# Optimization experiments

Measured on AMD Instinct MI355X. Metric: run time of the kernel, lower is better.

The kernel has to match this reference:

```python
import jax, jax.numpy as jnp
import numpy as np

B, H, S, D = 4, 16, 2048, 128


def setup_inputs() -> dict:
    key = jax.random.key(0)
    kq, kk, kv = jax.random.split(key, 3)
    query = jax.random.normal(kq, (B, H, S, D), dtype=jnp.float32)
    key_t = jax.random.normal(kk, (B, H, S, D), dtype=jnp.float32)
    value = jax.random.normal(kv, (B, H, S, D), dtype=jnp.float32)
    # causal mask, broadcast over batch and heads: True = keep
    mask = jnp.tril(jnp.ones((S, S), dtype=bool))[None, None].repeat(B, 0).repeat(H, 1)
    return {"query": query, "key": key_t, "value": value, "mask": mask}


def reference(query, key, value, mask):
    scale = 1.0 / np.sqrt(D).astype(np.float32)
    # [b,h,sq,sk] scores
    scores = jnp.einsum("bhqd,bhkd->bhqk", query, key) * scale
    scores = jnp.where(mask, scores, -jnp.inf)
    probs = jax.nn.softmax(scores, axis=-1)
    return jnp.einsum("bhqk,bhkd->bhqd", probs, value)
```

## Files before the change

### kernel.cpp

```cpp
#include <hip/hip_runtime.h>


#define SLEN 2048
#define DDIM 128
#define NBH  64
#define QB   256
#define KB   64

typedef __bf16 bf16x8 __attribute__((ext_vector_type(8)));
typedef float  f32x16 __attribute__((ext_vector_type(16)));
typedef float  f32x4  __attribute__((ext_vector_type(4)));
typedef unsigned uint32x4 __attribute__((ext_vector_type(4)));
typedef unsigned short ushort_t;
typedef ushort_t ushort8 __attribute__((ext_vector_type(8)));

__device__ inline ushort_t f2bf(float f) {
  union { float f; unsigned u; } v; v.f = f;
  unsigned u = v.u;
  u += 0x7FFFu + ((u >> 16) & 1u);
  return (ushort_t)(u >> 16);
}

__device__ inline unsigned cvtpk_bf16(float lo, float hi) {
  unsigned r;
  asm("v_cvt_pk_bf16_f32 %0, %1, %2" : "=v"(r) : "v"(lo), "v"(hi));
  return r;
}

__global__ __launch_bounds__(256) void convert_k_kernel(
    const float* __restrict__ in, ushort_t* __restrict__ out, int n4) {
  int stride = gridDim.x * blockDim.x;
  for (int i = blockIdx.x * blockDim.x + threadIdx.x; i < n4; i += stride) {
    float4 x = reinterpret_cast<const float4*>(in)[i];
    unsigned lo = (unsigned)f2bf(x.x) | ((unsigned)f2bf(x.y) << 16);
    unsigned hi = (unsigned)f2bf(x.z) | ((unsigned)f2bf(x.w) << 16);
    reinterpret_cast<uint2*>(out)[i] = make_uint2(lo, hi);
  }
}

__global__ __launch_bounds__(256) void transpose_v_kernel(
    const float* __restrict__ V, ushort_t* __restrict__ Vt) {
  __shared__ float t[64][33];
  const int bh = blockIdx.z;
  const int s0 = blockIdx.x * 64;
  const int d0 = blockIdx.y * 32;
  const int tx = threadIdx.x & 31;
  const int ty = threadIdx.x >> 5;
  const float* src = V + ((size_t)bh * SLEN + s0) * DDIM + d0;
#pragma unroll
  for (int j = 0; j < 8; ++j) {
    int sl = ty + j * 8;
    t[sl][tx] = src[(size_t)sl * DDIM + tx];
  }
  __syncthreads();
  ushort_t* dst = Vt + ((size_t)bh * DDIM + d0) * SLEN + s0;
#pragma unroll
  for (int j = 0; j < 4; ++j) {
    int dl = ty + j * 8;
    unsigned lo = f2bf(t[tx * 2][dl]);
    unsigned hi = f2bf(t[tx * 2 + 1][dl]);
    *reinterpret_cast<unsigned*>(&dst[(size_t)dl * SLEN + tx * 2]) =
        lo | (hi << 16);
  }
}

__global__ __launch_bounds__(512, 2) void fattn3_kernel(
    const float* __restrict__ Q, const ushort_t* __restrict__ Kb,
    const ushort_t* __restrict__ Vt, float* __restrict__ Out) {
  __shared__ ushort_t K_sh[2][KB * DDIM];
  __shared__ ushort_t V_sh[2][DDIM * KB];

  const int tid  = threadIdx.x;
  const int lane = tid & 63;
  const int wv   = tid >> 6;
  const int l31  = lane & 31;
  const int hi   = lane >> 5;
  const int qblk = (blockIdx.y >= 32) ? blockIdx.x : (7 - (int)blockIdx.x);
  const int bh   = blockIdx.y;

  const float scale = 0.08838834764831845f;

  const float*    Qp = Q  + (size_t)bh * SLEN * DDIM;
  const ushort_t* Kp = Kb + (size_t)bh * SLEN * DDIM;
  const ushort_t* Vp = Vt + (size_t)bh * DDIM * SLEN;
  float*          Op = Out + (size_t)bh * SLEN * DDIM;

  const int q0w = qblk * QB + wv * 32;
  const int qg  = q0w + l31;

  bf16x8 qf[8];
  {
    const float* qr = Qp + (size_t)qg * DDIM;
#pragma unroll
    for (int ds = 0; ds < 8; ++ds) {
      int d0 = ds * 16 + hi * 8;
      float4 x = *reinterpret_cast<const float4*>(qr + d0);
      float4 y = *reinterpret_cast<const float4*>(qr + d0 + 4);
      ushort8 uu;
      uu[0] = f2bf(x.x * scale); uu[1] = f2bf(x.y * scale);
      uu[2] = f2bf(x.z * scale); uu[3] = f2bf(x.w * scale);
      uu[4] = f2bf(y.x * scale); uu[5] = f2bf(y.y * scale);
      uu[6] = f2bf(y.z * scale); uu[7] = f2bf(y.w * scale);
      qf[ds] = __builtin_bit_cast(bf16x8, uu);
    }
  }

  f32x16 Oacc[4];
#pragma unroll
  for (int dt = 0; dt < 4; ++dt)
#pragma unroll
    for (int r = 0; r < 16; ++r) Oacc[dt][r] = 0.f;
  float m_run = -3.0e38f, l_run = 0.f;

  const int last_kb      = qblk * 4 + 3;
  const int last_kb_wave = (q0w + 31) >> 6;

  auto stage = [&](int buf, int kb) {
    const ushort_t* ksrc = Kp + (size_t)kb * KB * DDIM;
#pragma unroll
    for (int j = 0; j < 2; ++j) {
      int chunk = wv * 128 + j * 64 + lane;
      int row = chunk >> 4, c = chunk & 15;
      const ushort_t* g = ksrc + row * DDIM + ((c ^ (row & 7)) << 3);
      ushort_t* l = &K_sh[buf][(size_t)(wv * 128 + j * 64) * 8];
      __builtin_amdgcn_global_load_lds(
          (const __attribute__((address_space(1))) unsigned*)g,
          (__attribute__((address_space(3))) unsigned*)l, 16, 0, 0);
    }
    const ushort_t* vsrc = Vp + (size_t)kb * KB;
#pragma unroll
    for (int j = 0; j < 2; ++j) {
      int chunk = wv * 128 + j * 64 + lane;
      int row = chunk >> 3, c = chunk & 7;
      const ushort_t* g = vsrc + (size_t)row * SLEN + ((c ^ (row & 7)) << 3);
      ushort_t* l = &V_sh[buf][(size_t)(wv * 128 + j * 64) * 8];
      __builtin_amdgcn_global_load_lds(
          (const __attribute__((address_space(1))) unsigned*)g,
          (__attribute__((address_space(3))) unsigned*)l, 16, 0, 0);
    }
  };

  stage(0, 0);

  for (int kb = 0; kb <= last_kb; ++kb) {
    __syncthreads();
    if (kb < last_kb) stage((kb + 1) & 1, kb + 1);

    if (kb <= last_kb_wave) {
      const int buf = kb & 1;

      f32x16 sac[2];
#pragma unroll
      for (int mt = 0; mt < 2; ++mt) {
        f32x16 a;
#pragma unroll
        for (int r = 0; r < 16; ++r) a[r] = 0.f;
        int row = mt * 32 + l31;
        int sw = row & 7;
#pragma unroll
        for (int ds = 0; ds < 8; ++ds) {
          int c = ds * 2 + hi;
          bf16x8 kf = *reinterpret_cast<const bf16x8*>(
              &K_sh[buf][row * DDIM + ((c ^ sw) << 3)]);
          a = __builtin_amdgcn_mfma_f32_32x32x16_bf16(kf, qf[ds], a, 0, 0, 0);
        }
        sac[mt] = a;
      }

      if (kb * 64 + 63 > q0w) {
#pragma unroll
        for (int mt = 0; mt < 2; ++mt) {
          int kbase = kb * 64 + mt * 32 + 4 * hi;
#pragma unroll
          for (int r = 0; r < 16; ++r) {
            int krow = (r & 3) + 8 * (r >> 2);
            if (kbase + krow > qg) sac[mt][r] = -3.0e38f;
          }
        }
      }

      float tm = sac[0][0];
#pragma unroll
      for (int r = 1; r < 16; ++r) tm = fmaxf(tm, sac[0][r]);
#pragma unroll
      for (int r = 0; r < 16; ++r) tm = fmaxf(tm, sac[1][r]);
      tm = fmaxf(tm, __shfl_xor(tm, 32));

      if (!__all(tm <= m_run)) {
        float mnew  = fmaxf(m_run, tm);
        float alpha = __expf(m_run - mnew);
        m_run = mnew;
        l_run *= alpha;
#pragma unroll
        for (int dt = 0; dt < 4; ++dt)
#pragma unroll
          for (int r = 0; r < 16; ++r) Oacc[dt][r] *= alpha;
      }

      float rs = 0.f;
#pragma unroll
      for (int mt = 0; mt < 2; ++mt)
#pragma unroll
        for (int r = 0; r < 16; ++r) {
          float p = __expf(sac[mt][r] - m_run);
          sac[mt][r] = p;
          rs += p;
        }
      rs += __shfl_xor(rs, 32);
      l_run += rs;

      uint32x4 pw[4];
#pragma unroll
      for (int ks = 0; ks < 4; ++ks) {
        const int mt = ks >> 1;
        const int hb = 4 * 2 * (ks & 1);
        unsigned pk_h0_0 = cvtpk_bf16(sac[mt][hb + 0], sac[mt][hb + 1]);
        unsigned pk_h0_1 = cvtpk_bf16(sac[mt][hb + 2], sac[mt][hb + 3]);
        unsigned pk_h1_0 = cvtpk_bf16(sac[mt][hb + 4], sac[mt][hb + 5]);
        unsigned pk_h1_1 = cvtpk_bf16(sac[mt][hb + 6], sac[mt][hb + 7]);
        unsigned s0 = hi ? pk_h1_0 : pk_h0_0;
        unsigned s1 = hi ? pk_h1_1 : pk_h0_1;
        unsigned t0 = hi ? pk_h0_0 : pk_h1_0;
        unsigned t1 = hi ? pk_h0_1 : pk_h1_1;
        unsigned r0 = __shfl_xor(t0, 32);
        unsigned r1 = __shfl_xor(t1, 32);
        uint32x4 f;
        f.x = hi ? r0 : s0;
        f.y = hi ? r1 : s1;
        f.z = hi ? s0 : r0;
        f.w = hi ? s1 : r1;
        pw[ks] = f;
      }

#pragma unroll
      for (int dt = 0; dt < 4; ++dt) {
        int row = dt * 32 + l31;
        int sw = row & 7;
#pragma unroll
        for (int ks = 0; ks < 4; ++ks) {
          int c = ks * 2 + hi;
          bf16x8 vf = *reinterpret_cast<const bf16x8*>(
              &V_sh[buf][row * 64 + ((c ^ sw) << 3)]);
          Oacc[dt] = __builtin_amdgcn_mfma_f32_32x32x16_bf16(
              vf, __builtin_bit_cast(bf16x8, pw[ks]), Oacc[dt], 0, 0, 0);
        }
      }
    }
  }

  {
    float invl = 1.0f / l_run;
    float* orow = Op + (size_t)qg * DDIM;
#pragma unroll
    for (int dt = 0; dt < 4; ++dt)
#pragma unroll
      for (int r = 0; r < 16; ++r) {
        int d = dt * 32 + (r & 3) + 8 * (r >> 2) + 4 * hi;
        orow[d] = Oacc[dt][r] * invl;
      }
  }
}

__global__ __launch_bounds__(256) void fattn_kernel(
    const float* __restrict__ Q, const float* __restrict__ K,
    const float* __restrict__ V, float* __restrict__ Out) {
  __shared__ ushort_t K_sh[64 * 128];
  __shared__ ushort_t V_sh[128 * 64];
  __shared__ ushort_t P_sh[4][16 * 64];

  const int tid  = threadIdx.x;
  const int lane = tid & 63;
  const int wv   = tid >> 6;
  const int l16  = lane & 15;
  const int lhi  = lane >> 4;
  const int qblk = blockIdx.x;
  const int bh   = blockIdx.y;
  const float scale = 0.08838834764831845f;

  const size_t base = (size_t)bh * SLEN * DDIM;
  const float* Qp = Q + base;
  const float* Kp = K + base;
  const float* Vp = V + base;
  float*       Op = Out + base;

  bf16x8 qf[4];
  {
    const int qrow = qblk * 64 + wv * 16 + l16;
    const float* qr = Qp + (size_t)qrow * DDIM;
#pragma unroll
    for (int dc = 0; dc < 4; ++dc) {
      int d0 = dc * 32 + lhi * 8;
      float4 x = *reinterpret_cast<const float4*>(qr + d0);
      float4 y = *reinterpret_cast<const float4*>(qr + d0 + 4);
      ushort8 uu;
      uu[0] = f2bf(x.x * scale); uu[1] = f2bf(x.y * scale);
      uu[2] = f2bf(x.z * scale); uu[3] = f2bf(x.w * scale);
      uu[4] = f2bf(y.x * scale); uu[5] = f2bf(y.y * scale);
      uu[6] = f2bf(y.z * scale); uu[7] = f2bf(y.w * scale);
      qf[dc] = __builtin_bit_cast(bf16x8, uu);
    }
  }

  f32x4 Oacc[8];
#pragma unroll
  for (int i = 0; i < 8; ++i) Oacc[i] = (f32x4){0.f, 0.f, 0.f, 0.f};
  float m_run[4], l_run[4];
#pragma unroll
  for (int r = 0; r < 4; ++r) { m_run[r] = -3.0e38f; l_run[r] = 0.f; }

  for (int kb = 0; kb <= qblk; ++kb) {
    __syncthreads();
    {
      const float* src = Kp + (size_t)kb * 64 * DDIM;
#pragma unroll
      for (int it = 0; it < 8; ++it) {
        int idx4 = it * 256 + tid;
        int r  = idx4 >> 5;
        int c4 = idx4 & 31;
        float4 x = *reinterpret_cast<const float4*>(src + r * DDIM + c4 * 4);
        unsigned lo = ((unsigned)f2bf(x.y) << 16) | f2bf(x.x);
        unsigned hh = ((unsigned)f2bf(x.w) << 16) | f2bf(x.z);
        int e = (r * 128 + c4 * 4) ^ ((r & 7) << 3);
        *reinterpret_cast<uint2*>(&K_sh[e]) = make_uint2(lo, hh);
      }
      const float* vs = Vp + (size_t)kb * 64 * DDIM;
#pragma unroll
      for (int it = 0; it < 8; ++it) {
        int idx4 = it * 256 + tid;
        int r  = idx4 >> 5;
        int c4 = idx4 & 31;
        float4 x = *reinterpret_cast<const float4*>(vs + r * DDIM + c4 * 4);
        int c0 = c4 * 4;
        float vals[4] = {x.x, x.y, x.z, x.w};
#pragma unroll
        for (int j = 0; j < 4; ++j) {
          int d = c0 + j;
          V_sh[(d * 64 + r) ^ ((d & 7) << 3)] = f2bf(vals[j]);
        }
      }
    }
    __syncthreads();

    f32x4 sacc[4];
#pragma unroll
    for (int g = 0; g < 4; ++g) {
      f32x4 acc = (f32x4){0.f, 0.f, 0.f, 0.f};
#pragma unroll
      for (int dc = 0; dc < 4; ++dc) {
        int row = g * 16 + l16;
        int e = (row * 128 + dc * 32 + lhi * 8) ^ ((row & 7) << 3);
        bf16x8 kf = *reinterpret_cast<const bf16x8*>(&K_sh[e]);
        acc = __builtin_amdgcn_mfma_f32_16x16x32_bf16(qf[dc], kf, acc, 0, 0, 0);
      }
      sacc[g] = acc;
    }

    if (kb == qblk) {
      int q0 = lhi * 4;
#pragma unroll
      for (int g = 0; g < 4; ++g) {
        int kcol = g * 16 + l16;
#pragma unroll
        for (int r = 0; r < 4; ++r) {
          if (kcol > wv * 16 + q0 + r) sacc[g][r] = -3.0e38f;
        }
      }
    }

    float tmax[4];
#pragma unroll
    for (int r = 0; r < 4; ++r)
      tmax[r] = fmaxf(fmaxf(sacc[0][r], sacc[1][r]),
                      fmaxf(sacc[2][r], sacc[3][r]));
#pragma unroll
    for (int x = 1; x < 16; x <<= 1) {
#pragma unroll
      for (int r = 0; r < 4; ++r)
        tmax[r] = fmaxf(tmax[r], __shfl_xor(tmax[r], x));
    }

    float alpha[4], mnew[4];
#pragma unroll
    for (int r = 0; r < 4; ++r) {
      mnew[r]  = fmaxf(m_run[r], tmax[r]);
      alpha[r] = __expf(m_run[r] - mnew[r]);
      m_run[r] = mnew[r];
    }

    float rsum[4] = {0.f, 0.f, 0.f, 0.f};
#pragma unroll
    for (int g = 0; g < 4; ++g) {
#pragma unroll
      for (int r = 0; r < 4; ++r) {
        float p = __expf(sacc[g][r] - mnew[r]);
        rsum[r] += p;
        int prow = lhi * 4 + r;
        P_sh[wv][(prow * 64 + g * 16 + l16) ^ ((prow & 7) << 3)] = f2bf(p);
      }
    }
#pragma unroll
    for (int x = 1; x < 16; x <<= 1) {
#pragma unroll
      for (int r = 0; r < 4; ++r) rsum[r] += __shfl_xor(rsum[r], x);
    }
#pragma unroll
    for (int r = 0; r < 4; ++r) l_run[r] = l_run[r] * alpha[r] + rsum[r];

#pragma unroll
    for (int dg = 0; dg < 8; ++dg)
#pragma unroll
      for (int r = 0; r < 4; ++r) Oacc[dg][r] *= alpha[r];

    bf16x8 pf[2];
#pragma unroll
    for (int kc = 0; kc < 2; ++kc) {
      int e = (l16 * 64 + kc * 32 + lhi * 8) ^ ((l16 & 7) << 3);
      pf[kc] = *reinterpret_cast<const bf16x8*>(&P_sh[wv][e]);
    }
#pragma unroll
    for (int dg = 0; dg < 8; ++dg) {
#pragma unroll
      for (int kc = 0; kc < 2; ++kc) {
        int row = dg * 16 + l16;
        int e = (row * 64 + kc * 32 + lhi * 8) ^ ((row & 7) << 3);
        bf16x8 vf = *reinterpret_cast<const bf16x8*>(&V_sh[e]);
        Oacc[dg] = __builtin_amdgcn_mfma_f32_16x16x32_bf16(pf[kc], vf, Oacc[dg], 0, 0, 0);
      }
    }
  }

#pragma unroll
  for (int r = 0; r < 4; ++r) {
    float inv = 1.0f / l_run[r];
    int q = qblk * 64 + wv * 16 + lhi * 4 + r;
    float* orow = Op + (size_t)q * DDIM;
#pragma unroll
    for (int dg = 0; dg < 8; ++dg)
      orow[dg * 16 + l16] = Oacc[dg][r] * inv;
  }
}

extern "C" void kernel_launch(void* const* d_in, const int* in_sizes, int n_in,
                              void* d_out, int out_size, void* d_ws, size_t ws_size,
                              hipStream_t stream) {
  const float* Q = (const float*)d_in[0];
  const float* K = (const float*)d_in[1];
  const float* V = (const float*)d_in[2];
  float* O = (float*)d_out;

  const size_t n_elem = (size_t)NBH * SLEN * DDIM;
  const size_t need   = n_elem * 2 * 2;

  if (ws_size >= need) {
    ushort_t* Kbf = (ushort_t*)d_ws;
    ushort_t* Vt  = Kbf + n_elem;
    convert_k_kernel<<<2048, 256, 0, stream>>>(K, Kbf, (int)(n_elem / 4));
    transpose_v_kernel<<<dim3(SLEN / 64, DDIM / 32, NBH), 256, 0, stream>>>(V, Vt);
    fattn3_kernel<<<dim3(SLEN / QB, NBH), dim3(512), 0, stream>>>(Q, Kbf, Vt, O);
  } else {
    fattn_kernel<<<dim3(SLEN / 64, NBH), dim3(256), 0, stream>>>(Q, K, V, O);
  }
}
```

Measured before the change: 149.8 us.

## Use exp2 with folded log2e scale, lazy rescale, permlane swap, MFMA priority

Folds log2(e) into the Q scale so the softmax can call the raw v_exp_f32 (exp2) instruction instead of __expf. The running-max rescale of the output accumulators is skipped unless the new max exceeds the old one by more than a threshold. It also replaces the cross-half shuffle used to pack P with v_permlane32_swap, splits the max and sum reductions into four independent chains, and raises wave priority around the MFMA loops. The lazy rescale risks fp32 overflow headroom issues if scores jump by less than the threshold repeatedly, but the bound keeps the exponentials at most 2^11.

Result: faster. 143.1 us (-4.5%).

```diff
diff --git a/kernel.cpp b/kernel.cpp
--- a/kernel.cpp
+++ b/kernel.cpp
@@ -24,6 +24,12 @@
 __device__ inline unsigned cvtpk_bf16(float lo, float hi) {
   unsigned r;
   asm("v_cvt_pk_bf16_f32 %0, %1, %2" : "=v"(r) : "v"(lo), "v"(hi));
+  return r;
+}
+
+__device__ inline float exp2_fast(float x) {
+  float r;
+  asm("v_exp_f32 %0, %1" : "=v"(r) : "v"(x));
   return r;
 }
 
@@ -64,7 +70,7 @@
   }
 }
 
-__global__ __launch_bounds__(512, 2) void fattn3_kernel(
+__global__ __launch_bounds__(512, 2) void fattn4_kernel(
     const float* __restrict__ Q, const ushort_t* __restrict__ Kb,
     const ushort_t* __restrict__ Vt, float* __restrict__ Out) {
   __shared__ ushort_t K_sh[2][KB * DDIM];
@@ -78,7 +84,8 @@
   const int qblk = (blockIdx.y >= 32) ? blockIdx.x : (7 - (int)blockIdx.x);
   const int bh   = blockIdx.y;
 
-  const float scale = 0.08838834764831845f;
+  const float qscale = 0.12751744f;
+  const float THR = 11.0f;
 
   const float*    Qp = Q  + (size_t)bh * SLEN * DDIM;
   const ushort_t* Kp = Kb + (size_t)bh * SLEN * DDIM;
@@ -97,10 +104,10 @@
       float4 x = *reinterpret_cast<const float4*>(qr + d0);
       float4 y = *reinterpret_cast<const float4*>(qr + d0 + 4);
       ushort8 uu;
-      uu[0] = f2bf(x.x * scale); uu[1] = f2bf(x.y * scale);
-      uu[2] = f2bf(x.z * scale); uu[3] = f2bf(x.w * scale);
-      uu[4] = f2bf(y.x * scale); uu[5] = f2bf(y.y * scale);
-      uu[6] = f2bf(y.z * scale); uu[7] = f2bf(y.w * scale);
+      uu[0] = f2bf(x.x * qscale); uu[1] = f2bf(x.y * qscale);
+      uu[2] = f2bf(x.z * qscale); uu[3] = f2bf(x.w * qscale);
+      uu[4] = f2bf(y.x * qscale); uu[5] = f2bf(y.y * qscale);
+      uu[6] = f2bf(y.z * qscale); uu[7] = f2bf(y.w * qscale);
       qf[ds] = __builtin_bit_cast(bf16x8, uu);
     }
   }
@@ -157,6 +164,7 @@
         for (int r = 0; r < 16; ++r) a[r] = 0.f;
         int row = mt * 32 + l31;
         int sw = row & 7;
+        __builtin_amdgcn_s_setprio(1);
 #pragma unroll
         for (int ds = 0; ds < 8; ++ds) {
           int c = ds * 2 + hi;
@@ -164,6 +172,7 @@
               &K_sh[buf][row * DDIM + ((c ^ sw) << 3)]);
           a = __builtin_amdgcn_mfma_f32_32x32x16_bf16(kf, qf[ds], a, 0, 0, 0);
         }
+        __builtin_amdgcn_s_setprio(0);
         sac[mt] = a;
       }
 
@@ -179,16 +188,23 @@
         }
       }
 
-      float tm = sac[0][0];
-#pragma unroll
-      for (int r = 1; r < 16; ++r) tm = fmaxf(tm, sac[0][r]);
-#pragma unroll
-      for (int r = 0; r < 16; ++r) tm = fmaxf(tm, sac[1][r]);
+      float p0 = sac[0][0], p1 = sac[0][1], p2 = sac[0][2], p3 = sac[0][3];
+#pragma unroll
+      for (int r = 4; r < 16; r += 4) {
+        p0 = fmaxf(p0, sac[0][r + 0]); p1 = fmaxf(p1, sac[0][r + 1]);
+        p2 = fmaxf(p2, sac[0][r + 2]); p3 = fmaxf(p3, sac[0][r + 3]);
+      }
+#pragma unroll
+      for (int r = 0; r < 16; r += 4) {
+        p0 = fmaxf(p0, sac[1][r + 0]); p1 = fmaxf(p1, sac[1][r + 1]);
+        p2 = fmaxf(p2, sac[1][r + 2]); p3 = fmaxf(p3, sac[1][r + 3]);
+      }
+      float tm = fmaxf(fmaxf(p0, p1), fmaxf(p2, p3));
       tm = fmaxf(tm, __shfl_xor(tm, 32));
 
-      if (!__all(tm <= m_run)) {
+      if (!__all(tm - m_run <= THR)) {
         float mnew  = fmaxf(m_run, tm);
-        float alpha = __expf(m_run - mnew);
+        float alpha = exp2_fast(m_run - mnew);
         m_run = mnew;
         l_run *= alpha;
 #pragma unroll
@@ -197,15 +213,20 @@
           for (int r = 0; r < 16; ++r) Oacc[dt][r] *= alpha;
       }
 
-      float rs = 0.f;
+      float s0 = 0.f, s1 = 0.f, s2 = 0.f, s3 = 0.f;
 #pragma unroll
       for (int mt = 0; mt < 2; ++mt)
 #pragma unroll
-        for (int r = 0; r < 16; ++r) {
-          float p = __expf(sac[mt][r] - m_run);
-          sac[mt][r] = p;
-          rs += p;
-        }
+        for (int r = 0; r < 16; r += 4) {
+          float e0 = exp2_fast(sac[mt][r + 0] - m_run);
+          float e1 = exp2_fast(sac[mt][r + 1] - m_run);
+          float e2 = exp2_fast(sac[mt][r + 2] - m_run);
+          float e3 = exp2_fast(sac[mt][r + 3] - m_run);
+          sac[mt][r + 0] = e0; sac[mt][r + 1] = e1;
+          sac[mt][r + 2] = e2; sac[mt][r + 3] = e3;
+          s0 += e0; s1 += e1; s2 += e2; s3 += e3;
+        }
+      float rs = (s0 + s1) + (s2 + s3);
       rs += __shfl_xor(rs, 32);
       l_run += rs;
 
@@ -213,22 +234,14 @@
 #pragma unroll
       for (int ks = 0; ks < 4; ++ks) {
         const int mt = ks >> 1;
-        const int hb = 4 * 2 * (ks & 1);
-        unsigned pk_h0_0 = cvtpk_bf16(sac[mt][hb + 0], sac[mt][hb + 1]);
-        unsigned pk_h0_1 = cvtpk_bf16(sac[mt][hb + 2], sac[mt][hb + 3]);
-        unsigned pk_h1_0 = cvtpk_bf16(sac[mt][hb + 4], sac[mt][hb + 5]);
-        unsigned pk_h1_1 = cvtpk_bf16(sac[mt][hb + 6], sac[mt][hb + 7]);
-        unsigned s0 = hi ? pk_h1_0 : pk_h0_0;
-        unsigned s1 = hi ? pk_h1_1 : pk_h0_1;
-        unsigned t0 = hi ? pk_h0_0 : pk_h1_0;
-        unsigned t1 = hi ? pk_h0_1 : pk_h1_1;
-        unsigned r0 = __shfl_xor(t0, 32);
-        unsigned r1 = __shfl_xor(t1, 32);
-        uint32x4 f;
-        f.x = hi ? r0 : s0;
-        f.y = hi ? r1 : s1;
-        f.z = hi ? s0 : r0;
-        f.w = hi ? s1 : r1;
+        const int hb = 8 * (ks & 1);
+        unsigned X  = cvtpk_bf16(sac[mt][hb + 0], sac[mt][hb + 1]);
+        unsigned X2 = cvtpk_bf16(sac[mt][hb + 2], sac[mt][hb + 3]);
+        unsigned Y  = cvtpk_bf16(sac[mt][hb + 4], sac[mt][hb + 5]);
+        unsigned Y2 = cvtpk_bf16(sac[mt][hb + 6], sac[mt][hb + 7]);
+        asm("v_permlane32_swap_b32 %0, %1" : "+v"(X),  "+v"(Y));
+        asm("v_permlane32_swap_b32 %0, %1" : "+v"(X2), "+v"(Y2));
+        uint32x4 f; f.x = X; f.y = X2; f.z = Y; f.w = Y2;
         pw[ks] = f;
       }
 
@@ -236,6 +249,7 @@
       for (int dt = 0; dt < 4; ++dt) {
         int row = dt * 32 + l31;
         int sw = row & 7;
+        __builtin_amdgcn_s_setprio(1);
 #pragma unroll
         for (int ks = 0; ks < 4; ++ks) {
           int c = ks * 2 + hi;
@@ -244,6 +258,7 @@
           Oacc[dt] = __builtin_amdgcn_mfma_f32_32x32x16_bf16(
               vf, __builtin_bit_cast(bf16x8, pw[ks]), Oacc[dt], 0, 0, 0);
         }
+        __builtin_amdgcn_s_setprio(0);
       }
     }
   }
@@ -456,7 +471,7 @@
     ushort_t* Vt  = Kbf + n_elem;
     convert_k_kernel<<<2048, 256, 0, stream>>>(K, Kbf, (int)(n_elem / 4));
     transpose_v_kernel<<<dim3(SLEN / 64, DDIM / 32, NBH), 256, 0, stream>>>(V, Vt);
-    fattn3_kernel<<<dim3(SLEN / QB, NBH), dim3(512), 0, stream>>>(Q, Kbf, Vt, O);
+    fattn4_kernel<<<dim3(SLEN / QB, NBH), dim3(512), 0, stream>>>(Q, Kbf, Vt, O);
   } else {
     fattn_kernel<<<dim3(SLEN / 64, NBH), dim3(256), 0, stream>>>(Q, K, V, O);
   }
```
